# Kernel optimization log

Hardware: AMD Instinct MI355X
Metric: run time of the kernel (lower is better)

Reference implementation:

```python
import jax, jax.numpy as jnp
import numpy as np

B, S, H = 2, 2048, 1024
E_DYN, E_FIX = 8, 1
I_DYN, I_FIX = 512, 2048
TOP_K = 4
TOP_P = 0.75
JITTER_EPS = 0.1
CAPACITY_FACTOR = 1.25
MIN_CAPACITY = 4


def setup_inputs() -> dict:
    key = jax.random.key(0)
    k = jax.random.split(key, 8)
    sc = 0.02
    return {
        "hidden_states": jax.random.normal(k[0], (B, S, H), jnp.float32),
        "gate_w": jax.random.normal(k[1], (E_DYN + E_FIX, H), jnp.float32) * sc,
        "dyn_gate_w": jax.random.normal(k[2], (E_DYN, I_DYN, H), jnp.float32) * sc,
        "dyn_up_w": jax.random.normal(k[3], (E_DYN, I_DYN, H), jnp.float32) * sc,
        "dyn_down_w": jax.random.normal(k[4], (E_DYN, H, I_DYN), jnp.float32) * sc,
        "sh_gate_w": jax.random.normal(k[5], (E_FIX, I_FIX, H), jnp.float32) * sc,
        "sh_up_w": jax.random.normal(k[6], (E_FIX, I_FIX, H), jnp.float32) * sc,
        "sh_down_w": jax.random.normal(k[7], (E_FIX, H, I_FIX), jnp.float32) * sc,
    }


def _sparse_mixer(scores):
    # Inference path of audio_sparse_expert_mixer (training=False: no gumbel noise).
    T = scores.shape[0]
    rows = jnp.arange(T)
    masked_scores = scores
    mults, sels = [], []
    for _ in range(TOP_K):  # small fixed structural loop
        thr = jnp.max(masked_scores, axis=-1, keepdims=True)          # [T,1]
        sel = jnp.argmax(masked_scores, axis=-1)                       # [T]
        factor = jnp.maximum(jnp.abs(scores), jnp.abs(thr))
        jmask = (thr - scores) / factor > 2.0 * JITTER_EPS             # bool, no grad
        gates = jax.nn.softmax(jnp.where(jmask, -jnp.inf, masked_scores), axis=-1)
        mult = jnp.take_along_axis(gates, sel[:, None], axis=-1)[:, 0]
        masked_scores = masked_scores.at[rows, sel].set(-jnp.inf)
        mults.append(mult)
        sels.append(sel)
    return jnp.stack(mults, axis=-1), jnp.stack(sels, axis=-1)        # [T,K]


def reference(hidden_states, gate_w, dyn_gate_w, dyn_up_w, dyn_down_w, sh_gate_w, sh_up_w, sh_down_w):
    Bv, Sv, Hv = hidden_states.shape
    T = Bv * Sv
    x = hidden_states.reshape(T, Hv)
    full_logits = x @ gate_w.T                                         # [T, E_DYN+E_FIX]
    dyn_logits = full_logits[:, :E_DYN]

    # audio_dynamic_expert_selection: per-token dynamic expert count via top_p
    probs = jax.nn.softmax(dyn_logits, axis=-1)
    sorted_p = jnp.sort(probs, axis=-1)[:, ::-1]
    csum = jnp.cumsum(sorted_p, axis=-1)
    dyn_k = jnp.minimum(jnp.sum(csum < TOP_P, axis=-1) + 1, TOP_K)     # [T]

    mult, sel = _sparse_mixer(dyn_logits)                              # [T,K]
    slot_valid = jnp.arange(TOP_K)[None, :] < dyn_k[:, None]
    mult = jnp.where(slot_valid, mult, 0.0)

    # dense per-expert routing weights (scatter top-k multipliers, normalize)
    rows = jnp.arange(T)
    rw = jnp.zeros((T, E_DYN), x.dtype).at[rows[:, None], sel].add(mult)
    rw = rw / jnp.sum(rw, axis=-1, keepdims=True)

    # capacity-based expert dropping (_audio_expert_capacity)
    mask_dyn = (rw > 0).astype(jnp.int32)
    cap = max(int(np.ceil(T / E_DYN * CAPACITY_FACTOR)), MIN_CAPACITY)
    mask_dyn = mask_dyn * (jnp.cumsum(mask_dyn, axis=0) <= cap)
    expert_mask = jnp.concatenate([mask_dyn, jnp.ones((T, E_FIX), jnp.int32)], axis=-1)
    maskf = expert_mask.astype(x.dtype)

    # calculate_audio_global_routing_weight + router_weight * expert_mask
    gw = jax.nn.softmax(jnp.where(expert_mask == 0, -jnp.inf, full_logits), axis=-1)
    gd = rw * jnp.sum(gw[:, :E_DYN], axis=-1, keepdims=True)
    global_w = jnp.concatenate([gd, gw[:, E_DYN:]], axis=-1) * maskf   # [T, E_DYN+E_FIX]

    # dynamic experts (SwiGLU), dense reference over all experts; mask/weights zero out drops
    g = jnp.einsum('th,eih->tei', x, dyn_gate_w)
    u = jnp.einsum('th,eih->tei', x, dyn_up_w)
    y_dyn = jnp.einsum('tei,ehi->teh', jax.nn.silu(g) * u, dyn_down_w)
    out = jnp.einsum('te,teh->th', global_w[:, :E_DYN], y_dyn)

    # shared (fixed) experts applied to all tokens
    gs = jnp.einsum('th,fih->tfi', x, sh_gate_w)
    us = jnp.einsum('th,fih->tfi', x, sh_up_w)
    y_sh = jnp.einsum('tfi,fhi->tfh', jax.nn.silu(gs) * us, sh_down_w)
    out = out + jnp.einsum('tf,tfh->th', global_w[:, E_DYN:], y_sh)

    return out.reshape(Bv, Sv, Hv)
```

## Files before the change

kernel.cpp:

```cpp
#include <hip/hip_runtime.h>
#include <cstdint>

typedef __attribute__((ext_vector_type(8))) __bf16 bf16x8;
typedef __attribute__((ext_vector_type(4))) float f32x4;

static constexpr int T_TOK = 4096;
static constexpr int HDIM  = 1024;
static constexpr int NEXP  = 9;
static constexpr int EDYN  = 8;
static constexpr int IDYN_ = 512;
static constexpr int IFIX_ = 2048;
static constexpr int CAPE  = 640;

__device__ __forceinline__ unsigned short f2bf(float f) {
  unsigned u = __float_as_uint(f);
  u += 0x7fffu + ((u >> 16) & 1u);
  return (unsigned short)(u >> 16);
}

__device__ __forceinline__ void gl_lds16(const void* g, void* l) {
  __builtin_amdgcn_global_load_lds((const __attribute__((address_space(1))) void*)g,
                                   (__attribute__((address_space(3))) void*)l,
                                   16, 0, 0);
}

static constexpr int D0 = 1048576;
static constexpr int D1 = D0 + 1048576;
static constexpr int D2 = D1 + 1048576;
static constexpr int D3 = D2 + 524288;
static constexpr int D4 = D3 + 524288;
static constexpr int D5 = D4 + 524288;
__global__ void cvt_all_kernel(const float4* __restrict__ s1,
                               const float4* __restrict__ s2, const float4* __restrict__ s3,
                               const float4* __restrict__ s4, const float4* __restrict__ s5,
                               const float4* __restrict__ s6,
                               ushort4* __restrict__ d1,
                               ushort4* __restrict__ d2, ushort4* __restrict__ d3,
                               ushort4* __restrict__ d4, ushort4* __restrict__ d5,
                               ushort4* __restrict__ d6) {
  int stride = gridDim.x * blockDim.x;
  for (int i = blockIdx.x * blockDim.x + threadIdx.x; i < D5; i += stride) {
    const float4* s; ushort4* d; int off;
    if      (i < D0) { s = s1; d = d1; off = i; }
    else if (i < D1) { s = s2; d = d2; off = i - D0; }
    else if (i < D2) { s = s3; d = d3; off = i - D1; }
    else if (i < D3) { s = s4; d = d4; off = i - D2; }
    else if (i < D4) { s = s5; d = d5; off = i - D3; }
    else             { s = s6; d = d6; off = i - D4; }
    float4 f = s[off];
    d[off] = make_ushort4(f2bf(f.x), f2bf(f.y), f2bf(f.z), f2bf(f.w));
  }
}

__global__ __launch_bounds__(256)
void logits_routing_kernel(const float* __restrict__ x, const float* __restrict__ gw,
                           unsigned short* __restrict__ xb,
                           float* __restrict__ logits, float* __restrict__ rw,
                           int* __restrict__ mask) {
  int wave = threadIdx.x >> 6, lane = threadIdx.x & 63;
  int t = blockIdx.x * 4 + wave;
  if (t >= T_TOK) return;
  const float* xr = x + (size_t)t * HDIM;
  float acc[NEXP];
#pragma unroll
  for (int e = 0; e < NEXP; ++e) acc[e] = 0.f;
#pragma unroll
  for (int half = 0; half < 2; ++half) {
    const int h0 = half * 512 + lane * 8;
    float4 a = *(const float4*)(xr + h0);
    float4 b = *(const float4*)(xr + h0 + 4);
    float v[8] = {a.x, a.y, a.z, a.w, b.x, b.y, b.z, b.w};
    union { unsigned short us[8]; uint4 u4; } pk;
#pragma unroll
    for (int j = 0; j < 8; ++j) pk.us[j] = f2bf(v[j]);
    *(uint4*)(xb + (size_t)t * HDIM + h0) = pk.u4;
#pragma unroll
    for (int e = 0; e < NEXP; ++e) {
      float s = 0.f;
#pragma unroll
      for (int j = 0; j < 8; ++j) s += v[j] * gw[e * HDIM + h0 + j];
      acc[e] += s;
    }
  }
#pragma unroll
  for (int e = 0; e < NEXP; ++e) {
    float v = acc[e];
#pragma unroll
    for (int off = 32; off > 0; off >>= 1) v += __shfl_down(v, off, 64);
    acc[e] = v;
  }
  if (lane != 0) return;
  float s[EDYN];
#pragma unroll
  for (int e = 0; e < NEXP; ++e) logits[t * NEXP + e] = acc[e];
#pragma unroll
  for (int e = 0; e < EDYN; ++e) s[e] = acc[e];

  float m = s[0];
#pragma unroll
  for (int e = 1; e < EDYN; ++e) m = fmaxf(m, s[e]);
  float p[EDYN]; float psum = 0.f;
#pragma unroll
  for (int e = 0; e < EDYN; ++e) { p[e] = expf(s[e] - m); psum += p[e]; }
#pragma unroll
  for (int e = 0; e < EDYN; ++e) p[e] /= psum;
  float sp[EDYN];
#pragma unroll
  for (int e = 0; e < EDYN; ++e) sp[e] = p[e];
  for (int i = 1; i < EDYN; ++i) {
    float key = sp[i]; int j = i - 1;
    while (j >= 0 && sp[j] < key) { sp[j + 1] = sp[j]; --j; }
    sp[j + 1] = key;
  }
  float c = 0.f; int cnt = 0;
#pragma unroll
  for (int e = 0; e < EDYN; ++e) { c += sp[e]; cnt += (c < 0.75f) ? 1 : 0; }
  int dyn_k = cnt + 1; if (dyn_k > 4) dyn_k = 4;

  float ms[EDYN];
#pragma unroll
  for (int e = 0; e < EDYN; ++e) ms[e] = s[e];
  float mult[4]; int sel[4];
  for (int k = 0; k < 4; ++k) {
    float thr = ms[0]; int am = 0;
#pragma unroll
    for (int e = 1; e < EDYN; ++e) if (ms[e] > thr) { thr = ms[e]; am = e; }
    float vals[EDYN]; float mx = -INFINITY;
#pragma unroll
    for (int e = 0; e < EDYN; ++e) {
      float factor = fmaxf(fabsf(s[e]), fabsf(thr));
      float ratio = (thr - s[e]) / factor;
      float v = (ratio > 0.2f) ? -INFINITY : ms[e];
      vals[e] = v; mx = fmaxf(mx, v);
    }
    float sum = 0.f;
#pragma unroll
    for (int e = 0; e < EDYN; ++e) sum += expf(vals[e] - mx);
    mult[k] = expf(vals[am] - mx) / sum;
    sel[k] = am;
    ms[am] = -INFINITY;
  }
  float r[EDYN];
#pragma unroll
  for (int e = 0; e < EDYN; ++e) r[e] = 0.f;
  for (int k = 0; k < 4; ++k) if (k < dyn_k) r[sel[k]] += mult[k];
  float ssum = 0.f;
#pragma unroll
  for (int e = 0; e < EDYN; ++e) ssum += r[e];
#pragma unroll
  for (int e = 0; e < EDYN; ++e) {
    float v = r[e] / ssum;
    rw[t * EDYN + e] = v;
    mask[t * EDYN + e] = (v > 0.f) ? 1 : 0;
  }
}

__global__ __launch_bounds__(1024)
void capacity_kernel(int* __restrict__ mask, int* __restrict__ tok,
                     int* __restrict__ counts) {
  const int e = blockIdx.x;
  const int tid = threadIdx.x;
  const int lane = tid & 63, wave = tid >> 6;
  __shared__ int wsum[16];
  const int t0 = tid * 4;
  int bits[4]; int c = 0;
#pragma unroll
  for (int j = 0; j < 4; ++j) { bits[j] = mask[(t0 + j) * EDYN + e]; c += bits[j]; }
  int sc = c;
#pragma unroll
  for (int off = 1; off < 64; off <<= 1) {
    int v = __shfl_up(sc, off, 64);
    if (lane >= off) sc += v;
  }
  if (lane == 63) wsum[wave] = sc;
  __syncthreads();
  int wbase = 0;
  for (int w = 0; w < wave; ++w) wbase += wsum[w];
  int pos = wbase + sc - c;
#pragma unroll
  for (int j = 0; j < 4; ++j) {
    int keep = bits[j] && (pos < CAPE);
    if (keep) tok[e * CAPE + pos] = t0 + j;
    mask[(t0 + j) * EDYN + e] = keep;
    pos += bits[j];
  }
  int total = 0;
  for (int w = 0; w < 16; ++w) total += wsum[w];
  int cnt = total < CAPE ? total : CAPE;
  if (tid == 0) counts[e] = cnt;
  for (int r = cnt + tid; r < CAPE; r += 1024) tok[e * CAPE + r] = -1;
}

__global__ __launch_bounds__(256)
void final_gate_kernel(const float* __restrict__ logits, const int* __restrict__ mask,
                       const float* __restrict__ rw, float* __restrict__ gdyn,
                       float* __restrict__ wsh) {
  int t = blockIdx.x * blockDim.x + threadIdx.x;
  if (t >= T_TOK) return;
  float vals[NEXP]; float mx = -INFINITY;
  int mk[EDYN];
#pragma unroll
  for (int e = 0; e < EDYN; ++e) {
    mk[e] = mask[t * EDYN + e];
    vals[e] = mk[e] ? logits[t * NEXP + e] : -INFINITY;
    mx = fmaxf(mx, vals[e]);
  }
  vals[EDYN] = logits[t * NEXP + EDYN];
  mx = fmaxf(mx, vals[EDYN]);
  float ex[NEXP]; float sum = 0.f;
#pragma unroll
  for (int e = 0; e < NEXP; ++e) { ex[e] = expf(vals[e] - mx); sum += ex[e]; }
  float inv = 1.f / sum;
  float sd = 0.f;
#pragma unroll
  for (int e = 0; e < EDYN; ++e) sd += ex[e] * inv;
#pragma unroll
  for (int e = 0; e < EDYN; ++e)
    gdyn[t * EDYN + e] = mk[e] ? rw[t * EDYN + e] * sd : 0.f;
  wsh[t] = ex[EDYN] * inv;
}

template <bool GATHER>
__global__ __launch_bounds__(256)
void gemm_gateup_kernel(const unsigned short* __restrict__ xb,
                        const unsigned short* __restrict__ Wg,
                        const unsigned short* __restrict__ Wu,
                        unsigned short* __restrict__ act,
                        const int* __restrict__ toklist,
                        const int* __restrict__ counts,
                        int N, int K, int Mstride, int MT) {
  const int e = blockIdx.z;
  const int nid = blockIdx.x;
  const int m0 = (nid % MT) * 128;
  const int n0 = (nid / MT) * 64;
  if (GATHER) { if (m0 >= counts[e]) return; }

  const unsigned short* Wg_e = Wg + (size_t)e * N * K;
  const unsigned short* Wu_e = Wu + (size_t)e * N * K;
  unsigned short* act_e = act + (size_t)e * Mstride * N;
  const int* tok_e = toklist + e * CAPE;

  __shared__ __align__(16) unsigned short As[128 * 64];
  __shared__ __align__(16) unsigned short Bgs[64 * 64];
  __shared__ __align__(16) unsigned short Bus[64 * 64];

  const int tid = threadIdx.x;
  const int lane = tid & 63;
  const int wave = tid >> 6;
  const int wr = wave >> 1, wc = wave & 1;
  const int srow = tid >> 3;
  const int scol = (tid & 7) * 8;

  const unsigned short* a_src[4];
#pragma unroll
  for (int it = 0; it < 4; ++it) {
    int r = m0 + it * 32 + srow;
    int ridx = r;
    if (GATHER) { int tv = tok_e[r]; ridx = tv < 0 ? 0 : tv; }
    a_src[it] = xb + (size_t)ridx * K + scol;
  }
  const unsigned short* bg_src[2]; const unsigned short* bu_src[2];
#pragma unroll
  for (int it = 0; it < 2; ++it) {
    int r = n0 + it * 32 + srow;
    bg_src[it] = Wg_e + (size_t)r * K + scol;
    bu_src[it] = Wu_e + (size_t)r * K + scol;
  }

  f32x4 accg[4][2], accu[4][2];
#pragma unroll
  for (int i = 0; i < 4; ++i)
#pragma unroll
    for (int j = 0; j < 2; ++j) {
      f32x4 z = {0.f, 0.f, 0.f, 0.f};
      accg[i][j] = z; accu[i][j] = z;
    }

  for (int kt = 0; kt < K; kt += 64) {
#pragma unroll
    for (int it = 0; it < 4; ++it)
      gl_lds16(a_src[it] + kt, &As[it * 2048 + wave * 512]);
#pragma unroll
    for (int it = 0; it < 2; ++it) {
      gl_lds16(bg_src[it] + kt, &Bgs[it * 2048 + wave * 512]);
      gl_lds16(bu_src[it] + kt, &Bus[it * 2048 + wave * 512]);
    }
    __syncthreads();
#pragma unroll
    for (int kk = 0; kk < 2; ++kk) {
      const int ko = kk * 32 + (lane >> 4) * 8;
      bf16x8 a[4], bg[2], bu[2];
#pragma unroll
      for (int mi = 0; mi < 4; ++mi)
        a[mi] = *reinterpret_cast<const bf16x8*>(&As[(wr * 64 + mi * 16 + (lane & 15)) * 64 + ko]);
#pragma unroll
      for (int ni = 0; ni < 2; ++ni) {
        bg[ni] = *reinterpret_cast<const bf16x8*>(&Bgs[(wc * 32 + ni * 16 + (lane & 15)) * 64 + ko]);
        bu[ni] = *reinterpret_cast<const bf16x8*>(&Bus[(wc * 32 + ni * 16 + (lane & 15)) * 64 + ko]);
      }
#pragma unroll
      for (int mi = 0; mi < 4; ++mi)
#pragma unroll
        for (int ni = 0; ni < 2; ++ni) {
          accg[mi][ni] = __builtin_amdgcn_mfma_f32_16x16x32_bf16(a[mi], bg[ni], accg[mi][ni], 0, 0, 0);
          accu[mi][ni] = __builtin_amdgcn_mfma_f32_16x16x32_bf16(a[mi], bu[ni], accu[mi][ni], 0, 0, 0);
        }
    }
    __syncthreads();
  }

#pragma unroll
  for (int mi = 0; mi < 4; ++mi)
#pragma unroll
    for (int ni = 0; ni < 2; ++ni)
#pragma unroll
      for (int j = 0; j < 4; ++j) {
        int row = m0 + wr * 64 + mi * 16 + (lane >> 4) * 4 + j;
        int col = n0 + wc * 32 + ni * 16 + (lane & 15);
        float g = accg[mi][ni][j], u = accu[mi][ni][j];
        float v = (g / (1.f + __expf(-g))) * u;
        act_e[(size_t)row * N + col] = f2bf(v);
      }
}

template <bool DYN>
__global__ __launch_bounds__(256)
void gemm_down_kernel(const unsigned short* __restrict__ act,
                      const unsigned short* __restrict__ Wd,
                      float* __restrict__ out,
                      const int* __restrict__ toklist,
                      const int* __restrict__ counts,
                      const float* __restrict__ gdyn,
                      const float* __restrict__ wsh,
                      int N, int K, int Mstride, int MT) {
  const int e = blockIdx.z;
  const int nid = blockIdx.x;
  const int m0 = (nid % MT) * 128;
  const int n0 = (nid / MT) * 128;
  if (DYN) { if (m0 >= counts[e]) return; }

  const unsigned short* A_e = act + (size_t)e * Mstride * K;
  const unsigned short* Wd_e = Wd + (size_t)e * N * K;

  __shared__ __align__(16) unsigned short As[128 * 64];
  __shared__ __align__(16) unsigned short Bs[128 * 64];

  const int tid = threadIdx.x;
  const int lane = tid & 63;
  const int wave = tid >> 6;
  const int wr = wave >> 1, wc = wave & 1;
  const int srow = tid >> 3;
  const int scol = (tid & 7) * 8;

  const unsigned short* a_src[4]; const unsigned short* b_src[4];
#pragma unroll
  for (int it = 0; it < 4; ++it) {
    a_src[it] = A_e + (size_t)(m0 + it * 32 + srow) * K + scol;
    b_src[it] = Wd_e + (size_t)(n0 + it * 32 + srow) * K + scol;
  }

  f32x4 acc[4][4];
#pragma unroll
  for (int i = 0; i < 4; ++i)
#pragma unroll
    for (int j = 0; j < 4; ++j) { f32x4 z = {0.f, 0.f, 0.f, 0.f}; acc[i][j] = z; }

  for (int kt = 0; kt < K; kt += 64) {
#pragma unroll
    for (int it = 0; it < 4; ++it) {
      gl_lds16(a_src[it] + kt, &As[it * 2048 + wave * 512]);
      gl_lds16(b_src[it] + kt, &Bs[it * 2048 + wave * 512]);
    }
    __syncthreads();
#pragma unroll
    for (int kk = 0; kk < 2; ++kk) {
      const int ko = kk * 32 + (lane >> 4) * 8;
      bf16x8 a[4], b[4];
#pragma unroll
      for (int mi = 0; mi < 4; ++mi)
        a[mi] = *reinterpret_cast<const bf16x8*>(&As[(wr * 64 + mi * 16 + (lane & 15)) * 64 + ko]);
#pragma unroll
      for (int ni = 0; ni < 4; ++ni)
        b[ni] = *reinterpret_cast<const bf16x8*>(&Bs[(wc * 64 + ni * 16 + (lane & 15)) * 64 + ko]);
#pragma unroll
      for (int mi = 0; mi < 4; ++mi)
#pragma unroll
        for (int ni = 0; ni < 4; ++ni)
          acc[mi][ni] = __builtin_amdgcn_mfma_f32_16x16x32_bf16(a[mi], b[ni], acc[mi][ni], 0, 0, 0);
    }
    __syncthreads();
  }

#pragma unroll
  for (int mi = 0; mi < 4; ++mi)
#pragma unroll
    for (int ni = 0; ni < 4; ++ni)
#pragma unroll
      for (int j = 0; j < 4; ++j) {
        int row = m0 + wr * 64 + mi * 16 + (lane >> 4) * 4 + j;
        int col = n0 + wc * 64 + ni * 16 + (lane & 15);
        float v = acc[mi][ni][j];
        if (DYN) {
          int t = toklist[e * CAPE + row];
          if (t >= 0)
            atomicAdd(&out[(size_t)t * HDIM + col], gdyn[t * EDYN + e] * v);
        } else {
          out[(size_t)row * HDIM + col] = wsh[row] * v;
        }
      }
}

extern "C" void kernel_launch(void* const* d_in, const int* in_sizes, int n_in,
                              void* d_out, int out_size, void* d_ws, size_t ws_size,
                              hipStream_t stream) {
  const float* x   = (const float*)d_in[0];
  const float* gw  = (const float*)d_in[1];
  const float* wdg = (const float*)d_in[2];
  const float* wdu = (const float*)d_in[3];
  const float* wdd = (const float*)d_in[4];
  const float* wsg = (const float*)d_in[5];
  const float* wsu = (const float*)d_in[6];
  const float* wsd = (const float*)d_in[7];
  float* out = (float*)d_out;

  char* p = (char*)d_ws;
  auto alloc = [&](size_t bytes) {
    char* r = p; p += (bytes + 255) & ~(size_t)255; return r;
  };
  unsigned short* xb    = (unsigned short*)alloc((size_t)T_TOK * HDIM * 2);
  unsigned short* wdgb  = (unsigned short*)alloc((size_t)EDYN * IDYN_ * HDIM * 2);
  unsigned short* wdub  = (unsigned short*)alloc((size_t)EDYN * IDYN_ * HDIM * 2);
  unsigned short* wddb  = (unsigned short*)alloc((size_t)EDYN * HDIM * IDYN_ * 2);
  unsigned short* wsgb  = (unsigned short*)alloc((size_t)IFIX_ * HDIM * 2);
  unsigned short* wsub  = (unsigned short*)alloc((size_t)IFIX_ * HDIM * 2);
  unsigned short* wsdb  = (unsigned short*)alloc((size_t)HDIM * IFIX_ * 2);
  unsigned short* actsh = (unsigned short*)alloc((size_t)T_TOK * IFIX_ * 2);
  unsigned short* actdy = (unsigned short*)alloc((size_t)EDYN * CAPE * IDYN_ * 2);
  float* logits = (float*)alloc((size_t)T_TOK * NEXP * 4);
  float* rw     = (float*)alloc((size_t)T_TOK * EDYN * 4);
  int*   mask   = (int*)alloc((size_t)T_TOK * EDYN * 4);
  float* gdyn   = (float*)alloc((size_t)T_TOK * EDYN * 4);
  float* wshv   = (float*)alloc((size_t)T_TOK * 4);
  int*   counts = (int*)alloc(256);
  int*   tok    = (int*)alloc((size_t)EDYN * CAPE * 4);

  cvt_all_kernel<<<dim3(2048), dim3(256), 0, stream>>>(
      (const float4*)wdg, (const float4*)wdu, (const float4*)wdd,
      (const float4*)wsg, (const float4*)wsu, (const float4*)wsd,
      (ushort4*)wdgb, (ushort4*)wdub, (ushort4*)wddb,
      (ushort4*)wsgb, (ushort4*)wsub, (ushort4*)wsdb);

  logits_routing_kernel<<<dim3(T_TOK / 4), dim3(256), 0, stream>>>(x, gw, xb, logits, rw, mask);
  capacity_kernel<<<dim3(EDYN), dim3(1024), 0, stream>>>(mask, tok, counts);
  final_gate_kernel<<<dim3(T_TOK / 256), dim3(256), 0, stream>>>(logits, mask, rw, gdyn, wshv);

  gemm_gateup_kernel<false><<<dim3((T_TOK / 128) * (IFIX_ / 64), 1, 1), dim3(256), 0, stream>>>(
      xb, wsgb, wsub, actsh, tok, counts, IFIX_, HDIM, T_TOK, T_TOK / 128);
  gemm_down_kernel<false><<<dim3((T_TOK / 128) * (HDIM / 128), 1, 1), dim3(256), 0, stream>>>(
      actsh, wsdb, out, tok, counts, gdyn, wshv, HDIM, IFIX_, T_TOK, T_TOK / 128);
  gemm_gateup_kernel<true><<<dim3((CAPE / 128) * (IDYN_ / 64), 1, EDYN), dim3(256), 0, stream>>>(
      xb, wdgb, wdub, actdy, tok, counts, IDYN_, HDIM, CAPE, CAPE / 128);
  gemm_down_kernel<true><<<dim3((CAPE / 128) * (HDIM / 128), 1, EDYN), dim3(256), 0, stream>>>(
      actdy, wddb, out, tok, counts, gdyn, wshv, HDIM, IDYN_, CAPE, CAPE / 128);
}
```

Baseline: 334.6 us.

## Add 8-phase pipelined 256x128 gate/up GEMM for shared expert

Replaces the generic 128x64 gate/up GEMM for the shared expert with a dedicated kernel. It uses 512 threads, 256x128 tiles, 128KB of double-buffered LDS filled by direct global-to-LDS loads with swizzled addressing, and an 8-phase schedule that interleaves staging, LDS reads and MFMA with setprio and explicit waitcnt/barriers. The goal is more data reuse per tile and better overlap of memory with compute on the largest GEMM. The cost is a large LDS footprint that limits occupancy, and hand-tuned waitcnt counts that are fragile. The kernel launches 256 blocks, which is fewer than the CU count, so it relies on per-CU efficiency.

```diff
diff --git a/kernel.cpp b/kernel.cpp
--- a/kernel.cpp
+++ b/kernel.cpp
@@ -220,20 +220,134 @@
   wsh[t] = ex[EDYN] * inv;
 }
 
-template <bool GATHER>
+__global__ __launch_bounds__(512, 2)
+void gemm_gateup_8ph(const unsigned short* __restrict__ xb,
+                     const unsigned short* __restrict__ Wg,
+                     const unsigned short* __restrict__ Wu,
+                     unsigned short* __restrict__ act) {
+  extern __shared__ char lds[];
+  constexpr int NT = HDIM / 64;
+  const int tid  = threadIdx.x;
+  const int lane = tid & 63;
+  const int wid  = tid >> 6;
+  const int wrh  = wid >> 2;
+  const int wc   = wid & 3;
+  const int m0 = (blockIdx.x & 15) * 256;
+  const int n0 = (blockIdx.x >> 4) * 128;
+
+  const int srow = wid * 16 + (lane >> 2);
+  const int sb9  = (lane >> 5) & 1;
+  const int scl  = ((lane & 3) << 4) ^ (sb9 << 5);
+  const char* sA0 = (const char*)xb + (size_t)(m0 + srow) * 2048 + scl;
+  const char* sA1 = sA0 + (size_t)128 * 2048;
+  const char* sBg = (const char*)Wg + (size_t)(n0 + srow) * 2048 + scl;
+  const char* sBu = (const char*)Wu + (size_t)(n0 + srow) * 2048 + scl;
+  const int ldsW = wid * 1024;
+
+  const int rl  = lane & 15;
+  const int swz = ((lane >> 4) << 4) ^ ((rl & 8) << 2);
+  const int aRd = wrh * 16384 + rl * 64 + swz;
+  const int bRd = wc * 2048 + rl * 64 + swz;
+
+  f32x4 accg[8][2], accu[8][2];
+#pragma unroll
+  for (int i = 0; i < 8; ++i)
+#pragma unroll
+    for (int j = 0; j < 2; ++j) {
+      f32x4 z = {0.f, 0.f, 0.f, 0.f};
+      accg[i][j] = z; accu[i][j] = z;
+    }
+  bf16x8 aF[2][4][2];
+  bf16x8 bF[2][2];
+
+#define STAGE8(srcp, regoff)                                               \
+  if (ktN < NT) {                                                          \
+    gl_lds16((srcp) + (size_t)ktN * 128,       lds + nxt * 65536 + (regoff) + ldsW);          \
+    gl_lds16((srcp) + (size_t)ktN * 128 + 64,  lds + nxt * 65536 + (regoff) + 8192 + ldsW);   \
+  }
+#define LOAD_A8(h)                                                         \
+  _Pragma("unroll") for (int rf = 0; rf < 4; ++rf)                         \
+  _Pragma("unroll") for (int ks = 0; ks < 2; ++ks)                         \
+    aF[h][rf][ks] = *reinterpret_cast<const bf16x8*>(                      \
+      lds + cur * 65536 + aRd + ks * 8192 + (h) * 4096 + rf * 1024);
+#define LOAD_B8(off)                                                       \
+  _Pragma("unroll") for (int cf = 0; cf < 2; ++cf)                         \
+  _Pragma("unroll") for (int ks = 0; ks < 2; ++ks)                         \
+    bF[cf][ks] = *reinterpret_cast<const bf16x8*>(                         \
+      lds + cur * 65536 + (off) + bRd + ks * 8192 + cf * 1024);
+#define MFMA_PH8(h, ACC)                                                   \
+  __builtin_amdgcn_s_setprio(1);                                           \
+  _Pragma("unroll") for (int rf = 0; rf < 4; ++rf)                         \
+  _Pragma("unroll") for (int cf = 0; cf < 2; ++cf)                         \
+  _Pragma("unroll") for (int ks = 0; ks < 2; ++ks)                         \
+    ACC[(h) * 4 + rf][cf] = __builtin_amdgcn_mfma_f32_16x16x32_bf16(       \
+        aF[h][rf][ks], bF[cf][ks], ACC[(h) * 4 + rf][cf], 0, 0, 0);        \
+  __builtin_amdgcn_s_setprio(0);
+#define BAR8() __builtin_amdgcn_sched_barrier(0);                          \
+               __builtin_amdgcn_s_barrier();                               \
+               __builtin_amdgcn_sched_barrier(0);
+
+  {
+    const int ktN = 0, nxt = 0;
+    STAGE8(sA0, 0) STAGE8(sA1, 16384) STAGE8(sBg, 32768) STAGE8(sBu, 49152)
+  }
+  asm volatile("s_waitcnt vmcnt(0)" ::: "memory");
+  BAR8()
+
+  for (int j = 0; j < NT; ++j) {
+    const int cur = j & 1, nxt = cur ^ 1, ktN = j + 1;
+    STAGE8(sA0, 0)
+    LOAD_A8(0)
+    LOAD_B8(32768)
+    MFMA_PH8(0, accg)
+    BAR8()
+    STAGE8(sA1, 16384)
+    LOAD_A8(1)
+    MFMA_PH8(1, accg)
+    asm volatile("s_waitcnt vmcnt(4)" ::: "memory");
+    BAR8()
+    STAGE8(sBg, 32768)
+    LOAD_B8(49152)
+    MFMA_PH8(0, accu)
+    BAR8()
+    STAGE8(sBu, 49152)
+    MFMA_PH8(1, accu)
+    asm volatile("s_waitcnt vmcnt(2)" ::: "memory");
+    BAR8()
+  }
+
+#pragma unroll
+  for (int rf = 0; rf < 8; ++rf)
+#pragma unroll
+    for (int cf = 0; cf < 2; ++cf)
+#pragma unroll
+      for (int jj = 0; jj < 4; ++jj) {
+        int row = m0 + wrh * 128 + (rf >> 2) * 64 + (rf & 3) * 16 + ((lane >> 4) << 2) + jj;
+        int col = n0 + wc * 32 + cf * 16 + (lane & 15);
+        float g = accg[rf][cf][jj], u = accu[rf][cf][jj];
+        float v = (g / (1.f + __expf(-g))) * u;
+        act[(size_t)row * IFIX_ + col] = f2bf(v);
+      }
+#undef STAGE8
+#undef LOAD_A8
+#undef LOAD_B8
+#undef MFMA_PH8
+#undef BAR8
+}
+
 __global__ __launch_bounds__(256)
-void gemm_gateup_kernel(const unsigned short* __restrict__ xb,
-                        const unsigned short* __restrict__ Wg,
-                        const unsigned short* __restrict__ Wu,
-                        unsigned short* __restrict__ act,
-                        const int* __restrict__ toklist,
-                        const int* __restrict__ counts,
-                        int N, int K, int Mstride, int MT) {
+void gemm_gateup_dyn(const unsigned short* __restrict__ xb,
+                     const unsigned short* __restrict__ Wg,
+                     const unsigned short* __restrict__ Wu,
+                     unsigned short* __restrict__ act,
+                     const int* __restrict__ toklist,
+                     const int* __restrict__ counts,
+                     int N, int K, int Mstride, int MT) {
   const int e = blockIdx.z;
   const int nid = blockIdx.x;
   const int m0 = (nid % MT) * 128;
   const int n0 = (nid / MT) * 64;
-  if (GATHER) { if (m0 >= counts[e]) return; }
+  if (m0 >= counts[e]) return;
 
   const unsigned short* Wg_e = Wg + (size_t)e * N * K;
   const unsigned short* Wu_e = Wu + (size_t)e * N * K;
@@ -255,9 +369,8 @@
 #pragma unroll
   for (int it = 0; it < 4; ++it) {
     int r = m0 + it * 32 + srow;
-    int ridx = r;
-    if (GATHER) { int tv = tok_e[r]; ridx = tv < 0 ? 0 : tv; }
-    a_src[it] = xb + (size_t)ridx * K + scol;
+    int tv = tok_e[r];
+    a_src[it] = xb + (size_t)(tv < 0 ? 0 : tv) * K + scol;
   }
   const unsigned short* bg_src[2]; const unsigned short* bu_src[2];
 #pragma unroll
@@ -454,11 +567,10 @@
   capacity_kernel<<<dim3(EDYN), dim3(1024), 0, stream>>>(mask, tok, counts);
   final_gate_kernel<<<dim3(T_TOK / 256), dim3(256), 0, stream>>>(logits, mask, rw, gdyn, wshv);
 
-  gemm_gateup_kernel<false><<<dim3((T_TOK / 128) * (IFIX_ / 64), 1, 1), dim3(256), 0, stream>>>(
-      xb, wsgb, wsub, actsh, tok, counts, IFIX_, HDIM, T_TOK, T_TOK / 128);
+  gemm_gateup_8ph<<<dim3(256), dim3(512), 131072, stream>>>(xb, wsgb, wsub, actsh);
   gemm_down_kernel<false><<<dim3((T_TOK / 128) * (HDIM / 128), 1, 1), dim3(256), 0, stream>>>(
       actsh, wsdb, out, tok, counts, gdyn, wshv, HDIM, IFIX_, T_TOK, T_TOK / 128);
-  gemm_gateup_kernel<true><<<dim3((CAPE / 128) * (IDYN_ / 64), 1, EDYN), dim3(256), 0, stream>>>(
+  gemm_gateup_dyn<<<dim3((CAPE / 128) * (IDYN_ / 64), 1, EDYN), dim3(256), 0, stream>>>(
       xb, wdgb, wdub, actdy, tok, counts, IDYN_, HDIM, CAPE, CAPE / 128);
   gemm_down_kernel<true><<<dim3((CAPE / 128) * (HDIM / 128), 1, EDYN), dim3(256), 0, stream>>>(
       actdy, wddb, out, tok, counts, gdyn, wshv, HDIM, IDYN_, CAPE, CAPE / 128);
```

After: 317.6 us. -5.1%, faster.
